# Optimization experiments

Measured on AMD Instinct MI355X. Metric: run time of the kernel, lower is better.

The kernel has to match this reference:

```python
import jax, jax.numpy as jnp
import numpy as np

EPS = 1e-5  # BatchNorm1d default eps


def _bn(x):
    # BatchNorm1d(affine=False) in training mode: batch stats, biased variance
    m = x.mean(axis=0)
    v = ((x - m) ** 2).mean(axis=0)
    return (x - m) / jnp.sqrt(v + EPS)


def _gconv(x, A, W, b):
    # GraphConv with MeanAggregator: concat(x, A@x) @ W + b, ReLU
    agg = jnp.einsum('gnm,gmd->gnd', A, x)
    cat = jnp.concatenate([x, agg], axis=-1)
    return jax.nn.relu(jnp.einsum('gnd,df->gnf', cat, W) + b)


def setup_inputs() -> dict:
    key = jax.random.key(0)
    ks = jax.random.split(key, 16)
    B, C, H, Wd = 4, 32, 512, 512
    G, N, F = 512, 41, 576  # local graphs, 1+8+8*4 nodes, 3*4*(32+6)+120 feat
    d = {}
    d['inputs'] = jax.random.normal(ks[0], (B, C, H, Wd), jnp.float32)
    d['node_feats'] = jax.random.normal(ks[1], (G, N, F), jnp.float32)
    A = jax.random.uniform(ks[2], (G, N, N), jnp.float32)
    d['A'] = A / A.sum(-1, keepdims=True)  # row-normalized adjacency (mean agg)
    d['knn_inx'] = jax.random.randint(ks[3], (G, 8), 0, N)
    d['conv_w'] = jax.random.normal(ks[4], (6, C), jnp.float32) * 0.01
    d['conv_b'] = jnp.zeros((6,), jnp.float32)
    dims = [(2 * F, 512), (2 * 512, 256), (2 * 256, 128), (2 * 128, 64)]
    for i, (di, do) in enumerate(dims):
        d['W%d' % (i + 1)] = jax.random.normal(ks[5 + i], (di, do), jnp.float32) / np.float32(np.sqrt(di))
        d['b%d' % (i + 1)] = jnp.zeros((do,), jnp.float32)
    d['cls_w1'] = jax.random.normal(ks[10], (64, 32), jnp.float32) / 8.0
    d['cls_b1'] = jnp.zeros((32,), jnp.float32)
    d['prelu_a'] = jnp.full((32,), 0.25, jnp.float32)
    d['cls_w2'] = jax.random.normal(ks[11], (32, 2), jnp.float32) / np.float32(np.sqrt(32))
    d['cls_b2'] = jnp.zeros((2,), jnp.float32)
    return d


def reference(inputs, node_feats, A, knn_inx, conv_w, conv_b, W1, b1, W2, b2, W3, b3, W4, b4, cls_w1, cls_b1, prelu_a, cls_w2, cls_b2):
    # 1x1 conv: out_conv(inputs)
    pred_maps = jnp.einsum('bchw,oc->bohw', inputs, conv_w) + conv_b[None, :, None, None]
    # GCN over local graphs
    G, N, F = node_feats.shape
    x = _bn(node_feats.reshape(G * N, F)).reshape(G, N, F)
    x = _gconv(x, A, W1, b1)
    x = _gconv(x, A, W2, b2)
    x = _gconv(x, A, W3, b3)
    x = _gconv(x, A, W4, b4)
    # gather knn neighbor node features per graph -> edge features
    edge = jnp.take_along_axis(x, knn_inx[:, :, None], axis=1).reshape(-1, x.shape[-1])
    h = edge @ cls_w1 + cls_b1
    h = jnp.where(h >= 0, h, prelu_a * h)  # PReLU(32)
    gcn_pred = h @ cls_w2 + cls_b2  # [G*k, 2]
    return (pred_maps, gcn_pred)
```

## Files before the change

### kernel.cpp

```cpp
#include <hip/hip_runtime.h>
#include <hip/hip_bf16.h>


using f32x4 = __attribute__((ext_vector_type(4))) float;
using s16x8 = __attribute__((ext_vector_type(8))) short;

#define GN 20992
#define NFEAT 576
#define NGRAPH 512
#define NNODE 41
#define ASTR 44
#define NTMG 171

typedef __attribute__((address_space(1))) const unsigned int gas_u32;
typedef __attribute__((address_space(3))) unsigned int las_u32;

__device__ __forceinline__ void gl_lds16(const void* g, void* l) {
  __builtin_amdgcn_global_load_lds((gas_u32*)g, (las_u32*)l, 16, 0, 0);
}

__device__ __forceinline__ float dot41_f4(const float* __restrict__ Am,
                                          const float* __restrict__ pr) {
  float s0 = 0.f, s1 = 0.f, s2 = 0.f, s3 = 0.f;
#pragma unroll
  for (int q = 0; q < 10; ++q) {
    float4 a4 = *(const float4*)(Am + q * 4);
    s0 += a4.x * pr[q * 4];
    s1 += a4.y * pr[q * 4 + 1];
    s2 += a4.z * pr[q * 4 + 2];
    s3 += a4.w * pr[q * 4 + 3];
  }
  return ((s0 + s1) + (s2 + s3)) + Am[40] * pr[40];
}

__global__ __launch_bounds__(576) void front_kernel(
    const float* __restrict__ nf, float* __restrict__ partial,
    __hip_bfloat16* __restrict__ x0) {
  int c = threadIdx.x;
  int u = blockIdx.x;
  int r0 = u * 82;
  const float* src = nf + (size_t)r0 * NFEAT + c;
  __hip_bfloat16* dst = x0 + (size_t)r0 * NFEAT + c;
  float s = 0.f, s2 = 0.f;
#pragma unroll 4
  for (int r = 0; r < 82; ++r) {
    float v = src[(size_t)r * NFEAT];
    s += v; s2 += v * v;
    dst[(size_t)r * NFEAT] = __float2bfloat16(v);
  }
  partial[(size_t)u * 1152 + c] = s;
  partial[(size_t)u * 1152 + NFEAT + c] = s2;
}

__global__ __launch_bounds__(256) void reduce_kernel(
    const float* __restrict__ partial, float* __restrict__ statsbuf) {
  int t = blockIdx.x * 256 + threadIdx.x;
  if (t >= NFEAT) return;
  float s = 0.f, s2 = 0.f;
#pragma unroll 8
  for (int u = 0; u < 256; ++u) {
    s += partial[(size_t)u * 1152 + t];
    s2 += partial[(size_t)u * 1152 + NFEAT + t];
  }
  float m = s * (1.f / GN);
  float v = s2 * (1.f / GN) - m * m;
  float inv = rsqrtf(v + 1e-5f);
  statsbuf[t] = inv;
  statsbuf[NFEAT + t] = m * inv;
}

__global__ __launch_bounds__(256) void wt1_kernel(
    const float* __restrict__ W1, const float* __restrict__ b1,
    const float* __restrict__ statsbuf, __hip_bfloat16* __restrict__ B1,
    float* __restrict__ gbias,
    const float* __restrict__ W2, const float* __restrict__ W3,
    const float* __restrict__ W4,
    __hip_bfloat16* __restrict__ B2, __hip_bfloat16* __restrict__ B3,
    __hip_bfloat16* __restrict__ B4) {
  int u = blockIdx.x;
  int tid = threadIdx.x;
  if (u < 576) {
    __shared__ float T[32 * 33];
    int jt = u / 18, kt = u - jt * 18;
    int j0 = jt * 32, k0 = kt * 32;
    int h = (j0 >= 512) ? 1 : 0;
    const float* Wh = W1 + (size_t)(h * 576) * 512 + (j0 - h * 512);
    int r = tid >> 5, cc = tid & 31;
#pragma unroll
    for (int i = 0; i < 4; ++i)
      T[(r + i * 8) * 33 + cc] = Wh[(size_t)(k0 + r + i * 8) * 512 + cc];
    __syncthreads();
    float invv = statsbuf[k0 + cc];
#pragma unroll
    for (int i = 0; i < 4; ++i) {
      int rowh = (j0 - h * 512) + r + i * 8;
      int jp = (rowh >> 6) * 128 + h * 64 + (rowh & 63);
      B1[(size_t)jp * 576 + k0 + cc] =
          __float2bfloat16(T[cc * 33 + (r + i * 8)] * invv);
    }
  } else if (u < 580) {
    int j = (u - 576) * 256 + tid;
    int col = (j < 512) ? j : j - 512;
    const float* base = W1 + (size_t)((j < 512) ? 0 : 576) * 512 + col;
    float s = 0.f;
#pragma unroll 4
    for (int f = 0; f < NFEAT; ++f) s += statsbuf[NFEAT + f] * base[(size_t)f * 512];
    gbias[j] = ((j < 512) ? b1[j] : 0.f) - s;
  } else {
    __shared__ float T[32 * 33];
    int t = u - 580;
    const float* W; __hip_bfloat16* B; int K, N;
    if (t < 256)      { W = W2; B = B2; K = 512; N = 256; }
    else if (t < 320) { W = W3; B = B3; K = 256; N = 128; t -= 256; }
    else              { W = W4; B = B4; K = 128; N = 64;  t -= 320; }
    int tilesN = N >> 5;
    int perhalf = (K >> 5) * tilesN;
    int h = t / perhalf; t -= h * perhalf;
    int tk = t / tilesN, tn = t - tk * tilesN;
    int r = tid >> 5, cc = tid & 31;
    const float* Wh = W + (size_t)h * K * N;
#pragma unroll
    for (int i = 0; i < 4; ++i)
      T[(r + i * 8) * 33 + cc] = Wh[(size_t)(tk * 32 + r + i * 8) * N + tn * 32 + cc];
    __syncthreads();
#pragma unroll
    for (int i = 0; i < 4; ++i) {
      int row = tn * 32 + r + i * 8;
      int jp = (row >> 6) * 128 + h * 64 + (row & 63);
      B[(size_t)jp * K + tk * 32 + cc] =
          __float2bfloat16(T[cc * 33 + r + i * 8]);
    }
  }
}

__global__ __launch_bounds__(256) void gemmagg_kernel(
    const __hip_bfloat16* __restrict__ Xptr, const __hip_bfloat16* __restrict__ Bt,
    const float* __restrict__ biasL, const float* __restrict__ biasR,
    __hip_bfloat16* __restrict__ Yptr, int Nout, int K, int NTN, int convBase,
    const float* __restrict__ Aadj,
    const float* __restrict__ cinputs, const float* __restrict__ conv_w,
    const float* __restrict__ conv_b, float* __restrict__ cout) {
  __shared__ __align__(16) char smem[53136];
  short* AshD = (short*)smem;
  short* BshD = (short*)(smem + 16384);
  __hip_bfloat16* Psh = (__hip_bfloat16*)smem;
  float* Aash = (float*)(smem + 31488);

  int tid = threadIdx.x;
  int bid = blockIdx.x;
  int gemmBlocks = NTMG * NTN;

  if (bid >= gemmBlocks) {
    int p = (convBase + bid - gemmBlocks) * 256 + tid;
    int img = p >> 16, q = p & 65535;
    const float4* ip = (const float4*)cinputs + (size_t)img * 32 * 65536 + q;
    float4 acc[6];
#pragma unroll
    for (int o = 0; o < 6; ++o) { float b0 = conv_b[o]; acc[o] = make_float4(b0, b0, b0, b0); }
#pragma unroll 4
    for (int c = 0; c < 32; ++c) {
      float4 x = ip[(size_t)c * 65536];
#pragma unroll
      for (int o = 0; o < 6; ++o) {
        float wv = conv_w[o * 32 + c];
        acc[o].x += x.x * wv; acc[o].y += x.y * wv;
        acc[o].z += x.z * wv; acc[o].w += x.w * wv;
      }
    }
    float4* op = (float4*)cout + (size_t)img * 6 * 65536 + q;
#pragma unroll
    for (int o = 0; o < 6; ++o) op[(size_t)o * 65536] = acc[o];
    return;
  }

  int sg = bid / (NTN * 8);
  int rem = bid - sg * (NTN * 8);
  int Wm = NTMG - sg * 8; if (Wm > 8) Wm = 8;
  int mt = sg * 8 + rem % Wm;
  int nt = rem / Wm;
  int row0 = mt * 123;
  int g0 = mt * 3;
  int gcnt = NGRAPH - g0; if (gcnt > 3) gcnt = 3;

  int wave = tid >> 6, lane = tid & 63;
  int wm = wave >> 1, wn = wave & 1;
  int lr = lane & 15, kb = lane >> 4;

  f32x4 acc[4][4];
#pragma unroll
  for (int m = 0; m < 4; ++m)
#pragma unroll
    for (int n = 0; n < 4; ++n) acc[m][n] = (f32x4){0.f, 0.f, 0.f, 0.f};

  const short* Ag = (const short*)Xptr;
  const short* Bg = (const short*)Bt + (size_t)nt * 128 * K;

  int c0 = tid, c1 = tid + 256;
  int ar0 = c0 >> 2, ak0 = (((c0 & 3) ^ ((ar0 >> 1) & 3))) * 8;
  int ar1 = c1 >> 2, ak1 = (((c1 & 3) ^ ((ar1 >> 1) & 3))) * 8;
  int grow0 = row0 + ar0; if (grow0 > GN - 1) grow0 = GN - 1;
  int grow1 = row0 + ar1; if (grow1 > GN - 1) grow1 = GN - 1;

  int aoff[4], boff[4];
#pragma unroll
  for (int m = 0; m < 4; ++m) {
    int r = wm * 64 + m * 16 + lr;
    aoff[m] = r * 32 + ((((r >> 1) & 3) ^ kb) * 8);
  }
#pragma unroll
  for (int n = 0; n < 4; ++n) {
    int r = wn * 64 + n * 16 + lr;
    boff[n] = r * 32 + ((((r >> 1) & 3) ^ kb) * 8);
  }

  gl_lds16(Ag + (size_t)grow0 * K + ak0, &AshD[c0 * 8]);
  gl_lds16(Ag + (size_t)grow1 * K + ak1, &AshD[c1 * 8]);
  gl_lds16(Bg + (size_t)ar0 * K + ak0, &BshD[c0 * 8]);
  gl_lds16(Bg + (size_t)ar1 * K + ak1, &BshD[c1 * 8]);
  __syncthreads();

  int nkt = K >> 5;
  int cur = 0;
  for (int kt = 0; kt < nkt; ++kt) {
    if (kt + 1 < nkt) {
      int k1 = (kt + 1) * 32;
      int nxt = (cur ^ 1) * 4096;
      gl_lds16(Ag + (size_t)grow0 * K + k1 + ak0, &AshD[nxt + c0 * 8]);
      gl_lds16(Ag + (size_t)grow1 * K + k1 + ak1, &AshD[nxt + c1 * 8]);
      gl_lds16(Bg + (size_t)ar0 * K + k1 + ak0, &BshD[nxt + c0 * 8]);
      gl_lds16(Bg + (size_t)ar1 * K + k1 + ak1, &BshD[nxt + c1 * 8]);
    }
    int cb = cur * 4096;
    s16x8 af[4], bfr[4];
#pragma unroll
    for (int m = 0; m < 4; ++m) af[m] = *(const s16x8*)&AshD[cb + aoff[m]];
#pragma unroll
    for (int n = 0; n < 4; ++n) bfr[n] = *(const s16x8*)&BshD[cb + boff[n]];
#pragma unroll
    for (int m = 0; m < 4; ++m)
#pragma unroll
      for (int n = 0; n < 4; ++n)
        acc[m][n] = __builtin_amdgcn_mfma_f32_16x16x32_bf16(af[m], bfr[n], acc[m][n], 0, 0, 0);
    __syncthreads();
    cur ^= 1;
  }

  int rbase = (lane >> 4) * 4;
#pragma unroll
  for (int m = 0; m < 4; ++m) {
    int lrow = wm * 64 + m * 16 + rbase;
#pragma unroll
    for (int n = 0; n < 4; ++n) {
      int w = wn * 64 + n * 16 + lr;
      float bv = (w < 64) ? biasL[nt * 64 + w]
                          : (biasR ? biasR[nt * 64 + (w - 64)] : 0.f);
#pragma unroll
      for (int r = 0; r < 4; ++r)
        Psh[(size_t)(lrow + r) * 128 + w] = __float2bfloat16(acc[m][n][r] + bv);
    }
  }
  __syncthreads();

  {
    int tot = gcnt * (NNODE * NNODE);
    const float* Asrc = Aadj + (size_t)g0 * (NNODE * NNODE);
    for (int i = tid; i < tot; i += 256) {
      int row = i / NNODE, m = i - row * NNODE;
      Aash[row * ASTR + m] = Asrc[i];
    }
  }
  __syncthreads();

  int c = tid & 63, grp = tid >> 6;
  for (int g = 0; g < gcnt; ++g) {
    float pr[NNODE];
#pragma unroll
    for (int m = 0; m < NNODE; ++m)
      pr[m] = __bfloat162float(Psh[(size_t)(g * NNODE + m) * 128 + 64 + c]);
#pragma unroll 1
    for (int n = grp; n < NNODE; n += 4) {
      float aa = __bfloat162float(Psh[(size_t)(g * NNODE + n) * 128 + c])
               + dot41_f4(Aash + (g * NNODE + n) * ASTR, pr);
      aa = aa > 0.f ? aa : 0.f;
      Yptr[(size_t)(row0 + g * NNODE + n) * Nout + nt * 64 + c] = __float2bfloat16(aa);
    }
  }
}

__global__ __launch_bounds__(256) void gemm4cls_kernel(
    const __hip_bfloat16* __restrict__ X, const __hip_bfloat16* __restrict__ B4t,
    const float* __restrict__ b4, const float* __restrict__ Aadj,
    const int* __restrict__ knn, const float* __restrict__ w1,
    const float* __restrict__ cb1, const float* __restrict__ pa,
    const float* __restrict__ w2, const float* __restrict__ cb2,
    float* __restrict__ out) {
  __shared__ __align__(16) char smem[49152 + 21648 + 31488 + 8192 + 520];
  short* AshD = (short*)smem;
  short* Bsh  = (short*)(smem + 16384);
  __hip_bfloat16* Psh = (__hip_bfloat16*)smem;
  float* Aash = (float*)(smem + 49152);
  float* Ysh  = (float*)(smem + 49152 + 21648);
  float* Wsh  = (float*)(smem + 49152 + 21648 + 31488);
  float* cb   = (float*)(smem + 49152 + 21648 + 31488 + 8192);

  int tid = threadIdx.x;
  int blk = blockIdx.x;
  int g0 = blk * 3;
  int gcnt = NGRAPH - g0; if (gcnt > 3) gcnt = 3;
  int row0 = blk * 123;

  {
    int tot = gcnt * (NNODE * NNODE);
    const float* Asrc = Aadj + (size_t)g0 * (NNODE * NNODE);
    for (int i = tid; i < tot; i += 256) {
      int row = i / NNODE, m = i - row * NNODE;
      Aash[row * ASTR + m] = Asrc[i];
    }
  }
  for (int i = tid; i < 2048; i += 256) Wsh[i] = w1[i];
  if (tid < 32) { cb[tid] = cb1[tid]; cb[32 + tid] = pa[tid]; }
  if (tid < 64) cb[64 + tid] = w2[tid];
  if (tid < 2) cb[128 + tid] = cb2[tid];

#pragma unroll
  for (int i = 0; i < 8; ++i) {
    int c = tid + i * 256;
    int kt = c >> 9, w = c & 511;
    int r = w >> 2, kc = ((w & 3) ^ ((r >> 1) & 3)) * 8;
    gl_lds16((const short*)B4t + (size_t)r * 128 + kt * 32 + kc, &Bsh[c * 8]);
  }
  const short* Ag = (const short*)X;
  int c0 = tid, c1 = tid + 256;
  int ar0 = c0 >> 2, ak0 = (((c0 & 3) ^ ((ar0 >> 1) & 3))) * 8;
  int ar1 = c1 >> 2, ak1 = (((c1 & 3) ^ ((ar1 >> 1) & 3))) * 8;
  int grow0 = row0 + ar0; if (grow0 > GN - 1) grow0 = GN - 1;
  int grow1 = row0 + ar1; if (grow1 > GN - 1) grow1 = GN - 1;
  gl_lds16(Ag + (size_t)grow0 * 128 + ak0, &AshD[c0 * 8]);
  gl_lds16(Ag + (size_t)grow1 * 128 + ak1, &AshD[c1 * 8]);
  __syncthreads();

  int wave = tid >> 6, lane = tid & 63;
  int wm = wave >> 1, wn = wave & 1;
  int lr = lane & 15, kb = lane >> 4;
  int aoff[4], boff[4];
#pragma unroll
  for (int m = 0; m < 4; ++m) {
    int r = wm * 64 + m * 16 + lr;
    aoff[m] = r * 32 + ((((r >> 1) & 3) ^ kb) * 8);
  }
#pragma unroll
  for (int n = 0; n < 4; ++n) {
    int r = wn * 64 + n * 16 + lr;
    boff[n] = r * 32 + ((((r >> 1) & 3) ^ kb) * 8);
  }
  f32x4 acc[4][4];
#pragma unroll
  for (int m = 0; m < 4; ++m)
#pragma unroll
    for (int n = 0; n < 4; ++n) acc[m][n] = (f32x4){0.f, 0.f, 0.f, 0.f};

  int cur = 0;
  for (int kt = 0; kt < 4; ++kt) {
    if (kt < 3) {
      int k1 = (kt + 1) * 32;
      int nxt = (cur ^ 1) * 4096;
      gl_lds16(Ag + (size_t)grow0 * 128 + k1 + ak0, &AshD[nxt + c0 * 8]);
      gl_lds16(Ag + (size_t)grow1 * 128 + k1 + ak1, &AshD[nxt + c1 * 8]);
    }
    int cbse = cur * 4096;
    s16x8 af[4], bfr[4];
#pragma unroll
    for (int m = 0; m < 4; ++m) af[m] = *(const s16x8*)&AshD[cbse + aoff[m]];
#pragma unroll
    for (int n = 0; n < 4; ++n) bfr[n] = *(const s16x8*)&Bsh[kt * 4096 + boff[n]];
#pragma unroll
    for (int m = 0; m < 4; ++m)
#pragma unroll
      for (int n = 0; n < 4; ++n)
        acc[m][n] = __builtin_amdgcn_mfma_f32_16x16x32_bf16(af[m], bfr[n], acc[m][n], 0, 0, 0);
    __syncthreads();
    cur ^= 1;
  }
  int rbase = (lane >> 4) * 4;
#pragma unroll
  for (int m = 0; m < 4; ++m) {
    int lrow = wm * 64 + m * 16 + rbase;
#pragma unroll
    for (int n = 0; n < 4; ++n) {
      int col = wn * 64 + n * 16 + lr;
      float bv = (col < 64) ? b4[col] : 0.f;
#pragma unroll
      for (int r = 0; r < 4; ++r)
        Psh[(size_t)(lrow + r) * 128 + col] = __float2bfloat16(acc[m][n][r] + bv);
    }
  }
  __syncthreads();

  int c = tid & 63, grp = tid >> 6;
  for (int g = 0; g < gcnt; ++g) {
    float pr[NNODE];
#pragma unroll
    for (int m = 0; m < NNODE; ++m)
      pr[m] = __bfloat162float(Psh[(size_t)(g * NNODE + m) * 128 + 64 + c]);
#pragma unroll 1
    for (int n = grp; n < NNODE; n += 4) {
      float aa = __bfloat162float(Psh[(size_t)(g * NNODE + n) * 128 + c])
               + dot41_f4(Aash + (g * NNODE + n) * ASTR, pr);
      Ysh[(g * NNODE + n) * 64 + c] = aa > 0.f ? aa : 0.f;
    }
  }
  __syncthreads();

  int j = tid & 31, slot = tid >> 5;
  for (int el = slot; el < 8 * gcnt; el += 8) {
    int e = g0 * 8 + el;
    int node = knn[e];
    int gl = el >> 3;
    const float* fp = &Ysh[(gl * NNODE + node) * 64];
    float a2 = cb[j];
#pragma unroll
    for (int d = 0; d < 64; ++d) a2 += fp[d] * Wsh[d * 32 + j];
    float h = a2 >= 0.f ? a2 : cb[32 + j] * a2;
#pragma unroll
    for (int o = 0; o < 2; ++o) {
      float v = h * cb[64 + j * 2 + o];
      v += __shfl_xor(v, 16, 32); v += __shfl_xor(v, 8, 32);
      v += __shfl_xor(v, 4, 32);  v += __shfl_xor(v, 2, 32);
      v += __shfl_xor(v, 1, 32);
      if (j == 0) out[(size_t)e * 2 + o] = v;
    }
  }
}

extern "C" void kernel_launch(void* const* d_in, const int* in_sizes, int n_in,
                              void* d_out, int out_size, void* d_ws, size_t ws_size,
                              hipStream_t stream) {
  const float* inputs     = (const float*)d_in[0];
  const float* node_feats = (const float*)d_in[1];
  const float* Aadj       = (const float*)d_in[2];
  const int*   knn        = (const int*)d_in[3];
  const float* conv_w     = (const float*)d_in[4];
  const float* conv_b     = (const float*)d_in[5];
  const float* W1 = (const float*)d_in[6];  const float* b1 = (const float*)d_in[7];
  const float* W2 = (const float*)d_in[8];  const float* b2 = (const float*)d_in[9];
  const float* W3 = (const float*)d_in[10]; const float* b3 = (const float*)d_in[11];
  const float* W4 = (const float*)d_in[12]; const float* b4 = (const float*)d_in[13];
  const float* cls_w1 = (const float*)d_in[14]; const float* cls_b1 = (const float*)d_in[15];
  const float* prelu_a = (const float*)d_in[16];
  const float* cls_w2 = (const float*)d_in[17]; const float* cls_b2 = (const float*)d_in[18];
  float* out = (float*)d_out;

  char* ws = (char*)d_ws;
  char* R1 = ws;
  char* R2 = ws + 24200192;
  char* wp = ws + 24200192 + 42991616;
  __hip_bfloat16* B1t = (__hip_bfloat16*)wp;  wp += 1179648;
  __hip_bfloat16* B2t = (__hip_bfloat16*)wp;  wp += 524288;
  __hip_bfloat16* B3t = (__hip_bfloat16*)wp;  wp += 131072;
  __hip_bfloat16* B4t = (__hip_bfloat16*)wp;  wp += 32768;
  float* partial  = (float*)wp;               wp += 256 * 1152 * 4;
  float* statsbuf = (float*)wp;               wp += 1152 * 4;
  float* gbias    = (float*)wp;               wp += 1024 * 4;

  __hip_bfloat16* x0 = (__hip_bfloat16*)R1;

  front_kernel<<<256, 576, 0, stream>>>(node_feats, partial, x0);
  reduce_kernel<<<3, 256, 0, stream>>>(partial, statsbuf);
  wt1_kernel<<<932, 256, 0, stream>>>(W1, b1, statsbuf, B1t, gbias,
                                      W2, W3, W4, B2t, B3t, B4t);

  gemmagg_kernel<<<NTMG * 8, 256, 0, stream>>>(
      x0, B1t, gbias, gbias + 512, (__hip_bfloat16*)R2, 512, 576, 8, 0,
      Aadj, nullptr, nullptr, nullptr, nullptr);
  gemmagg_kernel<<<NTMG * 4 + 512, 256, 0, stream>>>(
      (__hip_bfloat16*)R2, B2t, b2, nullptr, (__hip_bfloat16*)R1, 256, 512, 4,
      0, Aadj, inputs, conv_w, conv_b, out);
  gemmagg_kernel<<<NTMG * 2 + 512, 256, 0, stream>>>(
      (__hip_bfloat16*)R1, B3t, b3, nullptr, (__hip_bfloat16*)R2, 128, 256, 2,
      512, Aadj, inputs, conv_w, conv_b, out);
  gemm4cls_kernel<<<171, 256, 0, stream>>>(
      (__hip_bfloat16*)R2, B4t, b4, Aadj, knn, cls_w1, cls_b1, prelu_a,
      cls_w2, cls_b2, out + 6291456);
}
```

Baseline: 240.5 us.

## Triple-buffer GEMM LDS tiles with explicit vmcnt waits and split barriers

Replaces the double-buffered K loop of the fused GEMM/aggregation kernel with a three-stage ring of LDS buffers, prefetching three K-tiles ahead. It uses manual s_waitcnt vmcnt levels and raw s_barrier calls wrapped in sched_barrier, instead of __syncthreads. The goal is to hide more global-to-LDS load latency behind the MFMA work. The B buffer region moves so it can hold three stages, which now overlaps the region used for the adjacency tile. The loop also has two barriers per iteration, and the hand-coded vmcnt counts assume no other vector memory operations are outstanding.

```diff
diff --git a/kernel.cpp b/kernel.cpp
--- a/kernel.cpp
+++ b/kernel.cpp
@@ -142,7 +142,7 @@
     const float* __restrict__ conv_b, float* __restrict__ cout) {
   __shared__ __align__(16) char smem[53136];
   short* AshD = (short*)smem;
-  short* BshD = (short*)(smem + 16384);
+  short* BshD = (short*)(smem + 24576);
   __hip_bfloat16* Psh = (__hip_bfloat16*)smem;
   float* Aash = (float*)(smem + 31488);
 
@@ -213,24 +213,26 @@
     boff[n] = r * 32 + ((((r >> 1) & 3) ^ kb) * 8);
   }
 
-  gl_lds16(Ag + (size_t)grow0 * K + ak0, &AshD[c0 * 8]);
-  gl_lds16(Ag + (size_t)grow1 * K + ak1, &AshD[c1 * 8]);
-  gl_lds16(Bg + (size_t)ar0 * K + ak0, &BshD[c0 * 8]);
-  gl_lds16(Bg + (size_t)ar1 * K + ak1, &BshD[c1 * 8]);
-  __syncthreads();
-
   int nkt = K >> 5;
-  int cur = 0;
+#pragma unroll
+  for (int s = 0; s < 3; ++s) {
+    int k0 = s * 32;
+    gl_lds16(Ag + (size_t)grow0 * K + k0 + ak0, &AshD[s * 4096 + c0 * 8]);
+    gl_lds16(Ag + (size_t)grow1 * K + k0 + ak1, &AshD[s * 4096 + c1 * 8]);
+    gl_lds16(Bg + (size_t)ar0 * K + k0 + ak0, &BshD[s * 4096 + c0 * 8]);
+    gl_lds16(Bg + (size_t)ar1 * K + k0 + ak1, &BshD[s * 4096 + c1 * 8]);
+  }
+
   for (int kt = 0; kt < nkt; ++kt) {
-    if (kt + 1 < nkt) {
-      int k1 = (kt + 1) * 32;
-      int nxt = (cur ^ 1) * 4096;
-      gl_lds16(Ag + (size_t)grow0 * K + k1 + ak0, &AshD[nxt + c0 * 8]);
-      gl_lds16(Ag + (size_t)grow1 * K + k1 + ak1, &AshD[nxt + c1 * 8]);
-      gl_lds16(Bg + (size_t)ar0 * K + k1 + ak0, &BshD[nxt + c0 * 8]);
-      gl_lds16(Bg + (size_t)ar1 * K + k1 + ak1, &BshD[nxt + c1 * 8]);
-    }
-    int cb = cur * 4096;
+    int remS = nkt - kt;
+    if (remS >= 3)      asm volatile("s_waitcnt vmcnt(8)" ::: "memory");
+    else if (remS == 2) asm volatile("s_waitcnt vmcnt(4)" ::: "memory");
+    else                asm volatile("s_waitcnt vmcnt(0)" ::: "memory");
+    __builtin_amdgcn_sched_barrier(0);
+    __builtin_amdgcn_s_barrier();
+    __builtin_amdgcn_sched_barrier(0);
+
+    int cb = (kt % 3) * 4096;
     s16x8 af[4], bfr[4];
 #pragma unroll
     for (int m = 0; m < 4; ++m) af[m] = *(const s16x8*)&AshD[cb + aoff[m]];
@@ -241,8 +243,17 @@
 #pragma unroll
       for (int n = 0; n < 4; ++n)
         acc[m][n] = __builtin_amdgcn_mfma_f32_16x16x32_bf16(af[m], bfr[n], acc[m][n], 0, 0, 0);
-    __syncthreads();
-    cur ^= 1;
+
+    __builtin_amdgcn_sched_barrier(0);
+    __builtin_amdgcn_s_barrier();
+    __builtin_amdgcn_sched_barrier(0);
+    if (kt + 3 < nkt) {
+      int k1 = (kt + 3) * 32;
+      gl_lds16(Ag + (size_t)grow0 * K + k1 + ak0, &AshD[cb + c0 * 8]);
+      gl_lds16(Ag + (size_t)grow1 * K + k1 + ak1, &AshD[cb + c1 * 8]);
+      gl_lds16(Bg + (size_t)ar0 * K + k1 + ak0, &BshD[cb + c0 * 8]);
+      gl_lds16(Bg + (size_t)ar1 * K + k1 + ak1, &BshD[cb + c1 * 8]);
+    }
   }
 
   int rbase = (lane >> 4) * 4;
```

Measured after the change: 236.8 us, median of 2. No clear change (-1.5%).
